# Optimization experiments

Hardware: AMD Instinct MI355X
Metric: run time of the kernel (lower is better)

## Reference

```python
import jax, jax.numpy as jnp
import numpy as np

N_PATCHES = 14  # per side -> 196 patches

def patchify(images, n_patches):
    # images: [n, c, h, w]; returns [n, n_patches**2, c*ps*ps] with flatten order (c, ph, pw)
    n, c, h, w = images.shape
    ps = h // n_patches
    x = images.reshape(n, c, n_patches, ps, n_patches, ps)
    x = x.transpose(0, 2, 4, 1, 3, 5)  # [n, np_i, np_j, c, ps, ps]
    return x.reshape(n, n_patches * n_patches, c * ps * ps)

def setup_inputs() -> dict:
    key = jax.random.key(0)
    k1, k2, k3, k4 = jax.random.split(key, 4)
    B, C, H, Wd = 64, 3, 224, 224
    input_d = C * (H // N_PATCHES) * (Wd // N_PATCHES)  # 768
    hidden_d = 768
    images = jax.random.normal(k1, (B, C, H, Wd), dtype=jnp.float32)
    W = jax.random.normal(k2, (hidden_d, input_d), dtype=jnp.float32) * (1.0 / np.sqrt(input_d))
    b = jax.random.normal(k3, (hidden_d,), dtype=jnp.float32) * 0.01
    class_token = jax.random.uniform(k4, (1, hidden_d), dtype=jnp.float32)
    return {"images": images, "W": W, "b": b, "class_token": class_token}

def reference(images, W, b, class_token):
    patches = patchify(images, N_PATCHES)               # [B, 196, 768]
    tokens = jnp.einsum('bpd,hd->bph', patches, W) + b  # linear_mapper
    B = tokens.shape[0]
    cls = jnp.broadcast_to(class_token[None, :, :], (B, 1, class_token.shape[-1]))
    return jnp.concatenate([cls, tokens], axis=1)       # [B, 197, hidden_d]
```

## Files before the change

### kernel.cpp

```cpp
#include <hip/hip_runtime.h>
#include <cstdint>
#include <cstddef>

#define NB    64
#define NPAT  196
#define MTOT  (NB*NPAT)
#define KTOT  768
#define NTOT  768

typedef float  f32x4  __attribute__((ext_vector_type(4)));
typedef __bf16 bf16x8 __attribute__((ext_vector_type(8)));

#define A_BLOCKS   4704
#define W_BLOCKS   288
#define CLS_BLOCKS 48

__global__ __launch_bounds__(256) void prep_kernel(
    const float* __restrict__ images, const float* __restrict__ Wm,
    const float* __restrict__ cls, float* __restrict__ out,
    __bf16* __restrict__ Abuf, __bf16* __restrict__ Wbuf) {
  const int bid = blockIdx.x;
  const int tid = threadIdx.x;
  if (bid < A_BLOCKS) {
    const int q  = bid * 256 + tid;
    const int m  = q / 96;
    const int kc = q - m * 96;
    const int bb = m / 196;
    const int p  = m - bb * 196;
    const int pi = p / 14;
    const int pj = p - pi * 14;
    const int c   = kc >> 5;
    const int ph  = (kc & 31) >> 1;
    const int pw0 = (kc & 1) << 3;
    const size_t src =
        ((size_t)((bb * 3 + c) * 224 + pi * 16 + ph)) * 224 + (size_t)(pj * 16 + pw0);
    const float4 v0 = *(const float4*)(images + src);
    const float4 v1 = *(const float4*)(images + src + 4);
    bf16x8 o;
    o[0] = (__bf16)v0.x; o[1] = (__bf16)v0.y; o[2] = (__bf16)v0.z; o[3] = (__bf16)v0.w;
    o[4] = (__bf16)v1.x; o[5] = (__bf16)v1.y; o[6] = (__bf16)v1.z; o[7] = (__bf16)v1.w;
    *(bf16x8*)(Abuf + (size_t)q * 8) = o;
  } else if (bid < A_BLOCKS + W_BLOCKS) {
    const int q = (bid - A_BLOCKS) * 256 + tid;
    const float4 v0 = *(const float4*)(Wm + (size_t)q * 8);
    const float4 v1 = *(const float4*)(Wm + (size_t)q * 8 + 4);
    bf16x8 o;
    o[0] = (__bf16)v0.x; o[1] = (__bf16)v0.y; o[2] = (__bf16)v0.z; o[3] = (__bf16)v0.w;
    o[4] = (__bf16)v1.x; o[5] = (__bf16)v1.y; o[6] = (__bf16)v1.z; o[7] = (__bf16)v1.w;
    *(bf16x8*)(Wbuf + (size_t)q * 8) = o;
  } else {
    const int t  = (bid - A_BLOCKS - W_BLOCKS) * 256 + tid;
    const int bb = t / 192;
    const int r  = t - bb * 192;
    const float4 v = *(const float4*)(cls + r * 4);
    *(float4*)(out + (size_t)bb * 197 * 768 + r * 4) = v;
  }
}

#define BM 128
#define BN 128
#define BK 32
#define NBLK_N 6

__device__ __forceinline__ void gload_lds16(const void* g, void* l) {
  __builtin_amdgcn_global_load_lds((__attribute__((address_space(1))) void*)(g),
                                   (__attribute__((address_space(3))) void*)(l),
                                   16, 0, 0);
}

__global__ __launch_bounds__(256) void gemm_kernel(
    const __bf16* __restrict__ A, const __bf16* __restrict__ Wb,
    const float* __restrict__ bias, float* __restrict__ out) {
  __shared__ __bf16 As[BM * BK];
  __shared__ __bf16 Bs[BN * BK];

  const int tid  = threadIdx.x;
  const int bx   = blockIdx.x;
  const int nblk = bx % NBLK_N;
  const int mblk = bx / NBLK_N;
  const int m0 = mblk * BM;
  const int n0 = nblk * BN;
  const int wave = tid >> 6;
  const int lane = tid & 63;
  const int wm = (wave & 1) * 64;
  const int wn = (wave >> 1) * 64;
  const int lrow = lane & 15;
  const int lq   = lane >> 4;

  f32x4 acc[4][4] = {};

  const int q0 = tid, q1 = tid + 256;
  const __bf16* pA0 = A  + (size_t)(m0 + (q0 >> 2)) * KTOT + (q0 & 3) * 8;
  const __bf16* pA1 = A  + (size_t)(m0 + (q1 >> 2)) * KTOT + (q1 & 3) * 8;
  const __bf16* pB0 = Wb + (size_t)(n0 + (q0 >> 2)) * KTOT + (q0 & 3) * 8;
  const __bf16* pB1 = Wb + (size_t)(n0 + (q1 >> 2)) * KTOT + (q1 & 3) * 8;
  __bf16* lA0 = &As[wave * 512];
  __bf16* lA1 = &As[2048 + wave * 512];
  __bf16* lB0 = &Bs[wave * 512];
  __bf16* lB1 = &Bs[2048 + wave * 512];

  for (int kt = 0; kt < KTOT / BK; ++kt) {
    gload_lds16(pA0, lA0);
    gload_lds16(pA1, lA1);
    gload_lds16(pB0, lB0);
    gload_lds16(pB1, lB1);
    pA0 += BK; pA1 += BK; pB0 += BK; pB1 += BK;
    __syncthreads();

    bf16x8 af[4], bf[4];
#pragma unroll
    for (int i = 0; i < 4; ++i)
      af[i] = *(const bf16x8*)&As[(wm + i * 16 + lrow) * BK + lq * 8];
#pragma unroll
    for (int j = 0; j < 4; ++j)
      bf[j] = *(const bf16x8*)&Bs[(wn + j * 16 + lrow) * BK + lq * 8];

#pragma unroll
    for (int i = 0; i < 4; ++i)
#pragma unroll
      for (int j = 0; j < 4; ++j)
        acc[i][j] = __builtin_amdgcn_mfma_f32_16x16x32_bf16(af[i], bf[j], acc[i][j], 0, 0, 0);

    __syncthreads();
  }

#pragma unroll
  for (int j = 0; j < 4; ++j) {
    const int h  = n0 + wn + j * 16 + lrow;
    const float bv = bias[h];
#pragma unroll
    for (int i = 0; i < 4; ++i) {
      const int mbase = m0 + wm + i * 16 + lq * 4;
#pragma unroll
      for (int r = 0; r < 4; ++r) {
        const int m  = mbase + r;
        const int bb = m / 196;
        const int p  = m - bb * 196;
        out[(size_t)(bb * 197 + 1 + p) * 768 + h] = acc[i][j][r] + bv;
      }
    }
  }
}

extern "C" void kernel_launch(void* const* d_in, const int* in_sizes, int n_in,
                              void* d_out, int out_size, void* d_ws, size_t ws_size,
                              hipStream_t stream) {
  const float* images = (const float*)d_in[0];
  const float* Wm     = (const float*)d_in[1];
  const float* b      = (const float*)d_in[2];
  const float* cls    = (const float*)d_in[3];
  float* out = (float*)d_out;

  __bf16* Abuf = (__bf16*)d_ws;
  __bf16* Wbuf = Abuf + (size_t)MTOT * KTOT;
  (void)in_sizes; (void)n_in; (void)out_size; (void)ws_size;

  prep_kernel<<<A_BLOCKS + W_BLOCKS + CLS_BLOCKS, 256, 0, stream>>>(
      images, Wm, cls, out, Abuf, Wbuf);
  gemm_kernel<<<(MTOT / BM) * NBLK_N, 256, 0, stream>>>(Abuf, Wbuf, b, out);
}
```

Baseline: 122.7 us.

## Move patchify gather into GEMM loads and shrink M tile to 64

The prep kernel now converts images to bf16 in their original NCHW layout with fully contiguous reads and writes. The patch gather moves into the GEMM's global-to-LDS loads, where per-lane pointers walk image rows using stride jumps. The GEMM tile becomes 64x128 with BK=64, split into two 32-wide LDS halves, which doubles the block count and halves per-wave accumulators. The aim is to remove the strided scatter in prep and raise occupancy, at the cost of less coalesced 16-byte A loads and more reloading of B per output element.

```diff
diff --git a/kernel.cpp b/kernel.cpp
--- a/kernel.cpp
+++ b/kernel.cpp
@@ -2,64 +2,51 @@
 #include <cstdint>
 #include <cstddef>
 
-#define NB    64
-#define NPAT  196
-#define MTOT  (NB*NPAT)
-#define KTOT  768
-#define NTOT  768
+#define MTOT 12544
+#define KTOT 768
+#define NTOT 768
 
 typedef float  f32x4  __attribute__((ext_vector_type(4)));
 typedef __bf16 bf16x8 __attribute__((ext_vector_type(8)));
 
-#define A_BLOCKS   4704
-#define W_BLOCKS   288
+#define IMG_ELEMS (64*3*224*224)
+#define W_ELEMS   (768*768)
+#define A_BLOCKS  (IMG_ELEMS/8/256)
+#define W_BLOCKS  (W_ELEMS/8/256)
 #define CLS_BLOCKS 48
 
 __global__ __launch_bounds__(256) void prep_kernel(
     const float* __restrict__ images, const float* __restrict__ Wm,
     const float* __restrict__ cls, float* __restrict__ out,
-    __bf16* __restrict__ Abuf, __bf16* __restrict__ Wbuf) {
-  const int bid = blockIdx.x;
-  const int tid = threadIdx.x;
+    __bf16* __restrict__ imgb, __bf16* __restrict__ Wb) {
+  const int bid = blockIdx.x, tid = threadIdx.x;
   if (bid < A_BLOCKS) {
-    const int q  = bid * 256 + tid;
-    const int m  = q / 96;
-    const int kc = q - m * 96;
-    const int bb = m / 196;
-    const int p  = m - bb * 196;
-    const int pi = p / 14;
-    const int pj = p - pi * 14;
-    const int c   = kc >> 5;
-    const int ph  = (kc & 31) >> 1;
-    const int pw0 = (kc & 1) << 3;
-    const size_t src =
-        ((size_t)((bb * 3 + c) * 224 + pi * 16 + ph)) * 224 + (size_t)(pj * 16 + pw0);
-    const float4 v0 = *(const float4*)(images + src);
-    const float4 v1 = *(const float4*)(images + src + 4);
+    const size_t q = (size_t)bid * 256 + tid;
+    const float4 v0 = *(const float4*)(images + q * 8);
+    const float4 v1 = *(const float4*)(images + q * 8 + 4);
     bf16x8 o;
-    o[0] = (__bf16)v0.x; o[1] = (__bf16)v0.y; o[2] = (__bf16)v0.z; o[3] = (__bf16)v0.w;
-    o[4] = (__bf16)v1.x; o[5] = (__bf16)v1.y; o[6] = (__bf16)v1.z; o[7] = (__bf16)v1.w;
-    *(bf16x8*)(Abuf + (size_t)q * 8) = o;
+    o[0]=(__bf16)v0.x; o[1]=(__bf16)v0.y; o[2]=(__bf16)v0.z; o[3]=(__bf16)v0.w;
+    o[4]=(__bf16)v1.x; o[5]=(__bf16)v1.y; o[6]=(__bf16)v1.z; o[7]=(__bf16)v1.w;
+    *(bf16x8*)(imgb + q * 8) = o;
   } else if (bid < A_BLOCKS + W_BLOCKS) {
-    const int q = (bid - A_BLOCKS) * 256 + tid;
-    const float4 v0 = *(const float4*)(Wm + (size_t)q * 8);
-    const float4 v1 = *(const float4*)(Wm + (size_t)q * 8 + 4);
+    const size_t q = (size_t)(bid - A_BLOCKS) * 256 + tid;
+    const float4 v0 = *(const float4*)(Wm + q * 8);
+    const float4 v1 = *(const float4*)(Wm + q * 8 + 4);
     bf16x8 o;
-    o[0] = (__bf16)v0.x; o[1] = (__bf16)v0.y; o[2] = (__bf16)v0.z; o[3] = (__bf16)v0.w;
-    o[4] = (__bf16)v1.x; o[5] = (__bf16)v1.y; o[6] = (__bf16)v1.z; o[7] = (__bf16)v1.w;
-    *(bf16x8*)(Wbuf + (size_t)q * 8) = o;
+    o[0]=(__bf16)v0.x; o[1]=(__bf16)v0.y; o[2]=(__bf16)v0.z; o[3]=(__bf16)v0.w;
+    o[4]=(__bf16)v1.x; o[5]=(__bf16)v1.y; o[6]=(__bf16)v1.z; o[7]=(__bf16)v1.w;
+    *(bf16x8*)(Wb + q * 8) = o;
   } else {
     const int t  = (bid - A_BLOCKS - W_BLOCKS) * 256 + tid;
     const int bb = t / 192;
     const int r  = t - bb * 192;
-    const float4 v = *(const float4*)(cls + r * 4);
-    *(float4*)(out + (size_t)bb * 197 * 768 + r * 4) = v;
+    *(float4*)(out + (size_t)bb * 197 * 768 + r * 4) = *(const float4*)(cls + r * 4);
   }
 }
 
-#define BM 128
+#define BM 64
 #define BN 128
-#define BK 32
+#define BK 64
 #define NBLK_N 6
 
 __device__ __forceinline__ void gload_lds16(const void* g, void* l) {
@@ -69,58 +56,78 @@
 }
 
 __global__ __launch_bounds__(256) void gemm_kernel(
-    const __bf16* __restrict__ A, const __bf16* __restrict__ Wb,
+    const __bf16* __restrict__ imgb, const __bf16* __restrict__ Wb,
     const float* __restrict__ bias, float* __restrict__ out) {
-  __shared__ __bf16 As[BM * BK];
-  __shared__ __bf16 Bs[BN * BK];
+  __shared__ __bf16 As[2 * 64 * 32];
+  __shared__ __bf16 Bs[2 * 128 * 32];
 
   const int tid  = threadIdx.x;
   const int bx   = blockIdx.x;
-  const int nblk = bx % NBLK_N;
   const int mblk = bx / NBLK_N;
+  const int nblk = bx - mblk * NBLK_N;
   const int m0 = mblk * BM;
   const int n0 = nblk * BN;
-  const int wave = tid >> 6;
-  const int lane = tid & 63;
-  const int wm = (wave & 1) * 64;
+  const int wave = tid >> 6, lane = tid & 63;
+  const int wm = (wave & 1) * 32;
   const int wn = (wave >> 1) * 64;
-  const int lrow = lane & 15;
-  const int lq   = lane >> 4;
+  const int lrow = lane & 15, lq = lane >> 4;
 
-  f32x4 acc[4][4] = {};
+  f32x4 acc[2][4] = {};
 
-  const int q0 = tid, q1 = tid + 256;
-  const __bf16* pA0 = A  + (size_t)(m0 + (q0 >> 2)) * KTOT + (q0 & 3) * 8;
-  const __bf16* pA1 = A  + (size_t)(m0 + (q1 >> 2)) * KTOT + (q1 & 3) * 8;
-  const __bf16* pB0 = Wb + (size_t)(n0 + (q0 >> 2)) * KTOT + (q0 & 3) * 8;
-  const __bf16* pB1 = Wb + (size_t)(n0 + (q1 >> 2)) * KTOT + (q1 & 3) * 8;
-  __bf16* lA0 = &As[wave * 512];
-  __bf16* lA1 = &As[2048 + wave * 512];
-  __bf16* lB0 = &Bs[wave * 512];
-  __bf16* lB1 = &Bs[2048 + wave * 512];
+  const __bf16* pA[2];
+#pragma unroll
+  for (int s = 0; s < 2; ++s) {
+    const int c = wave * 128 + s * 64 + lane;
+    const int kstep = c >> 8, rem = c & 255;
+    const int row = rem >> 2, jc = rem & 3;
+    const int m = m0 + row;
+    const int bb = m / 196, p = m - bb * 196;
+    const int pi = p / 14, pj = p - pi * 14;
+    const int ph_off = kstep * 2 + (jc >> 1);
+    const int pw_off = (jc & 1) * 8;
+    const size_t e = ((size_t)(bb * 3 * 224 + pi * 16 + ph_off)) * 224 + pj * 16 + pw_off;
+    pA[s] = imgb + e;
+  }
+  const __bf16* pB[4];
+#pragma unroll
+  for (int s = 0; s < 4; ++s) {
+    const int c = wave * 256 + s * 64 + lane;
+    const int kstep = c >> 9, rem = c & 511;
+    const int h = rem >> 2, jc = rem & 3;
+    pB[s] = Wb + (size_t)(n0 + h) * 768 + kstep * 32 + jc * 8;
+  }
+  __bf16* lA[2];
+  __bf16* lB[4];
+#pragma unroll
+  for (int s = 0; s < 2; ++s) lA[s] = As + (wave * 128 + s * 64) * 8;
+#pragma unroll
+  for (int s = 0; s < 4; ++s) lB[s] = Bs + (wave * 256 + s * 64) * 8;
 
   for (int kt = 0; kt < KTOT / BK; ++kt) {
-    gload_lds16(pA0, lA0);
-    gload_lds16(pA1, lA1);
-    gload_lds16(pB0, lB0);
-    gload_lds16(pB1, lB1);
-    pA0 += BK; pA1 += BK; pB0 += BK; pB1 += BK;
+#pragma unroll
+    for (int s = 0; s < 2; ++s) gload_lds16(pA[s], lA[s]);
+#pragma unroll
+    for (int s = 0; s < 4; ++s) gload_lds16(pB[s], lB[s]);
+    const int dA = ((kt & 3) == 3) ? 47488 : 896;
+    pA[0] += dA; pA[1] += dA;
+    pB[0] += BK; pB[1] += BK; pB[2] += BK; pB[3] += BK;
     __syncthreads();
 
-    bf16x8 af[4], bf[4];
 #pragma unroll
-    for (int i = 0; i < 4; ++i)
-      af[i] = *(const bf16x8*)&As[(wm + i * 16 + lrow) * BK + lq * 8];
+    for (int ks = 0; ks < 2; ++ks) {
+      bf16x8 af[2], bf[4];
 #pragma unroll
-    for (int j = 0; j < 4; ++j)
-      bf[j] = *(const bf16x8*)&Bs[(wn + j * 16 + lrow) * BK + lq * 8];
-
-#pragma unroll
-    for (int i = 0; i < 4; ++i)
+      for (int i = 0; i < 2; ++i)
+        af[i] = *(const bf16x8*)&As[ks * 2048 + (wm + i * 16 + lrow) * 32 + lq * 8];
 #pragma unroll
       for (int j = 0; j < 4; ++j)
-        acc[i][j] = __builtin_amdgcn_mfma_f32_16x16x32_bf16(af[i], bf[j], acc[i][j], 0, 0, 0);
-
+        bf[j] = *(const bf16x8*)&Bs[ks * 4096 + (wn + j * 16 + lrow) * 32 + lq * 8];
+#pragma unroll
+      for (int i = 0; i < 2; ++i)
+#pragma unroll
+        for (int j = 0; j < 4; ++j)
+          acc[i][j] = __builtin_amdgcn_mfma_f32_16x16x32_bf16(af[i], bf[j], acc[i][j], 0, 0, 0);
+    }
     __syncthreads();
   }
 
@@ -129,13 +136,12 @@
     const int h  = n0 + wn + j * 16 + lrow;
     const float bv = bias[h];
 #pragma unroll
-    for (int i = 0; i < 4; ++i) {
-      const int mbase = m0 + wm + i * 16 + lq * 4;
+    for (int i = 0; i < 2; ++i) {
+      const int mb = m0 + wm + i * 16 + lq * 4;
 #pragma unroll
       for (int r = 0; r < 4; ++r) {
-        const int m  = mbase + r;
-        const int bb = m / 196;
-        const int p  = m - bb * 196;
+        const int m  = mb + r;
+        const int bb = m / 196, p = m - bb * 196;
         out[(size_t)(bb * 197 + 1 + p) * 768 + h] = acc[i][j][r] + bv;
       }
     }
@@ -151,11 +157,11 @@
   const float* cls    = (const float*)d_in[3];
   float* out = (float*)d_out;
 
-  __bf16* Abuf = (__bf16*)d_ws;
-  __bf16* Wbuf = Abuf + (size_t)MTOT * KTOT;
+  __bf16* imgb = (__bf16*)d_ws;
+  __bf16* Wb   = imgb + (size_t)IMG_ELEMS;
   (void)in_sizes; (void)n_in; (void)out_size; (void)ws_size;
 
   prep_kernel<<<A_BLOCKS + W_BLOCKS + CLS_BLOCKS, 256, 0, stream>>>(
-      images, Wm, cls, out, Abuf, Wbuf);
-  gemm_kernel<<<(MTOT / BM) * NBLK_N, 256, 0, stream>>>(Abuf, Wbuf, b, out);
+      images, Wm, cls, out, imgb, Wb);
+  gemm_kernel<<<(MTOT / BM) * NBLK_N, 256, 0, stream>>>(imgb, Wb, b, out);
 }
```

Result: faster. 118.3 us (-3.6%).
